# Optimization experiments

Measured on AMD Instinct MI355X. Metric: run time of the kernel, lower is better.

## Reference

```python
import jax, jax.numpy as jnp
import numpy as np

N_NODES = 100_000
N_EDGES = 1_600_000
F_IN = 128
HID = 64
C_OUT = 16


def setup_inputs() -> dict:
    key = jax.random.key(0)
    k1, k2, k3, k4, k5 = jax.random.split(key, 5)
    x = jax.random.normal(k1, (N_NODES, F_IN), dtype=jnp.float32)
    edge_index = jax.random.randint(k2, (2, N_EDGES), 0, N_NODES, dtype=jnp.int64)
    edge_weight = jax.random.uniform(k3, (N_EDGES,), dtype=jnp.float32)
    # Glorot-ish init for the two GCNConv linear layers; PyG inits bias to zero.
    W1 = jax.random.normal(k4, (F_IN, HID), dtype=jnp.float32) * (1.0 / np.sqrt(F_IN))
    b1 = jnp.zeros((HID,), dtype=jnp.float32)
    W2 = jax.random.normal(k5, (HID, C_OUT), dtype=jnp.float32) * (1.0 / np.sqrt(HID))
    b2 = jnp.zeros((C_OUT,), dtype=jnp.float32)
    return {"x": x, "edge_index": edge_index, "edge_weight": edge_weight,
            "W1": W1, "b1": b1, "W2": W2, "b2": b2}


def gcn_layer(x, row, col, ew, W, b, n):
    """PyG GCNConv: h = D^-1/2 (A + I) D^-1/2 (x W) + b, with edge weights.
    Self loops (weight 1) are handled analytically instead of appending edges."""
    h = x @ W  # [n, out]
    deg = jax.ops.segment_sum(ew, col, num_segments=n) + 1.0  # +1 for self loop
    dinv = jax.lax.rsqrt(deg)  # deg >= 1 always
    norm = dinv[row] * ew * dinv[col]  # [E]
    agg = jax.ops.segment_sum(norm[:, None] * h[row], col, num_segments=n)
    return agg + (dinv * dinv)[:, None] * h + b


def reference(x, edge_index, edge_weight, W1, b1, W2, b2):
    row, col = edge_index[0], edge_index[1]
    h = jax.nn.relu(gcn_layer(x, row, col, edge_weight, W1, b1, N_NODES))
    # delete_min_weighted_edges(node=0): remove the min-weight edge with source 0.
    # Zeroing its weight is mathematically identical to deleting it (it then
    # contributes 0 to both the degree and the aggregation).
    masked = jnp.where(row == 0, edge_weight, jnp.inf)
    idx = jnp.argmin(masked)
    ew2 = edge_weight.at[idx].set(0.0)
    return gcn_layer(h, row, col, ew2, W2, b2, N_NODES)
```

## Files before the change

### kernel.cpp

```cpp
#include <hip/hip_runtime.h>
#include <hip/hip_bf16.h>
#include <stdint.h>

#define NN 100000
#define NE 1600000
#define FIN 128
#define HID 64
#define COUT 16

#define BUKSH 8
#define NBUK ((NN + 255) >> BUKSH)
#define PART_NB 512
#define EPB (NE / PART_NB)
#define TSLCAP 5632

typedef unsigned long long u64;
typedef short bf16x8 __attribute__((ext_vector_type(8)));
typedef float f32x4 __attribute__((ext_vector_type(4)));

struct Flags { int f32; int i64; };

__device__ __forceinline__ float b2f(__hip_bfloat16 v) { return __bfloat162float(v); }

__device__ __forceinline__ float ldf(const void* p, size_t i, int f32) {
    return f32 ? ((const float*)p)[i]
               : __bfloat162float(((const __hip_bfloat16*)p)[i]);
}
__device__ __forceinline__ int lde(const void* p, size_t i, int i64) {
    return i64 ? (int)((const long long*)p)[i] : ((const int*)p)[i];
}
__device__ __forceinline__ void ld4bf(const __hip_bfloat16* p, float& x0, float& x1,
                                      float& x2, float& x3) {
    union { uint2 u; __hip_bfloat16 h[4]; } v;
    v.u = *(const uint2*)p;
    x0 = b2f(v.h[0]); x1 = b2f(v.h[1]); x2 = b2f(v.h[2]); x3 = b2f(v.h[3]);
}
__device__ __forceinline__ unsigned short f2bfu(float f) {
    union { __hip_bfloat16 b; unsigned short u; } c;
    c.b = __float2bfloat16(f);
    return c.u;
}
__device__ __forceinline__ float bfu2f(unsigned short u) {
    union { unsigned short h[2]; float f; } c;
    c.h[0] = 0; c.h[1] = u;
    return c.f;
}

__global__ __launch_bounds__(64) void k_init(const unsigned short* xs,
                                             const int* ei32, Flags* fl,
                                             u64* minkey, int* delpos,
                                             int* rowptrN) {
    int lane = threadIdx.x;
    int huge = 0;
    for (int i = lane * 2; i < 1024; i += 128) {
        int e = (xs[i] >> 7) & 0xFF;
        if (e >= 0xC0) huge = 1;
    }
    int odd_nonzero = 0;
    for (int i = 1 + lane * 2; i < 512; i += 128) {
        if (ei32[i] != 0) odd_nonzero = 1;
    }
    u64 h = __ballot(huge), o = __ballot(odd_nonzero);
    if (lane == 0) {
        fl->f32 = (h != 0); fl->i64 = (o == 0);
        *minkey = ~0ull;
        *delpos = 0x7fffffff;
        rowptrN[NN] = NE;
    }
}

__global__ __launch_bounds__(512) void k_hist(const void* __restrict__ ei,
                                              const void* __restrict__ ew,
                                              const Flags* __restrict__ fl,
                                              int* __restrict__ blockhist,
                                              u64* __restrict__ minkey) {
    __shared__ int cnt[NBUK];
    int b = blockIdx.x, t = threadIdx.x;
    int f32 = fl->f32, i64 = fl->i64;
    for (int i = t; i < NBUK; i += 512) cnt[i] = 0;
    __syncthreads();
    int e0 = b * EPB;
    for (int i = t; i < EPB; i += 512) {
        int e = e0 + i;
        int c = lde(ei, (size_t)NE + e, i64);
        atomicAdd(&cnt[c >> BUKSH], 1);
        int r = lde(ei, (size_t)e, i64);
        if (r == 0) {
            float w = ldf(ew, e, f32);
            u64 key = ((u64)__float_as_uint(w) << 32) | (unsigned)e;
            atomicMin(minkey, key);
        }
    }
    __syncthreads();
    for (int i = t; i < NBUK; i += 512)
        blockhist[(size_t)b * NBUK + i] = cnt[i];
}

__global__ __launch_bounds__(256) void k_scan1(const int* __restrict__ blockhist,
                                               int* __restrict__ buktotal) {
    __shared__ int sm[256];
    int i = blockIdx.x, t = threadIdx.x;
    int s = 0;
    for (int b = t; b < PART_NB; b += 256) s += blockhist[(size_t)b * NBUK + i];
    sm[t] = s;
    __syncthreads();
    for (int off = 128; off > 0; off >>= 1) {
        if (t < off) sm[t] += sm[t + off];
        __syncthreads();
    }
    if (t == 0) buktotal[i] = sm[0];
}

__global__ __launch_bounds__(512) void k_scan2(const int* __restrict__ blockhist,
                                               const int* __restrict__ buktotal,
                                               int* __restrict__ blockbase,
                                               int* __restrict__ bucketBaseArr) {
    __shared__ int pfx[512];
    __shared__ int bbs;
    int i = blockIdx.x, t = threadIdx.x;
    pfx[t] = (t < i && t < NBUK) ? buktotal[t] : 0;
    __syncthreads();
    for (int off = 256; off > 0; off >>= 1) {
        if (t < off) pfx[t] += pfx[t + off];
        __syncthreads();
    }
    if (t == 0) { bbs = pfx[0]; bucketBaseArr[i] = pfx[0]; }
    __syncthreads();
    int gbase = bbs;
    __syncthreads();
    int v = blockhist[(size_t)t * NBUK + i];
    pfx[t] = v;
    for (int off = 1; off < 512; off <<= 1) {
        __syncthreads();
        int add = (t >= off) ? pfx[t - off] : 0;
        __syncthreads();
        pfx[t] += add;
    }
    __syncthreads();
    blockbase[(size_t)t * NBUK + i] = gbase + pfx[t] - v;
}

__global__ __launch_bounds__(512) void k_scat(const void* __restrict__ ei,
                                              const void* __restrict__ ew,
                                              const Flags* __restrict__ fl,
                                              const int* __restrict__ blockbase,
                                              long long* __restrict__ tmp) {
    __shared__ int cnt[NBUK];
    int b = blockIdx.x, t = threadIdx.x;
    int f32 = fl->f32, i64 = fl->i64;
    for (int i = t; i < NBUK; i += 512) cnt[i] = 0;
    __syncthreads();
    int e0 = b * EPB;
    const int* bb = blockbase + (size_t)b * NBUK;
    for (int i = t; i < EPB; i += 512) {
        int e = e0 + i;
        int c = lde(ei, (size_t)NE + e, i64);
        int r = lde(ei, (size_t)e, i64);
        float w = ldf(ew, e, f32);
        int buk = c >> BUKSH;
        int local = atomicAdd(&cnt[buk], 1);
        int pos = bb[buk] + local;
        unsigned lo = (unsigned)r | (((unsigned)c & 255u) << 17);
        tmp[pos] = ((long long)__float_as_int(w) << 32) | lo;
    }
}

__global__ __launch_bounds__(512) void k_partB(const int* __restrict__ buktotal,
                                               const int* __restrict__ bucketBaseArr,
                                               const long long* __restrict__ tmp,
                                               int2* __restrict__ epack,
                                               int* __restrict__ rowptrN,
                                               const void* __restrict__ ei,
                                               const void* __restrict__ ew,
                                               const Flags* __restrict__ fl,
                                               const u64* __restrict__ minkey,
                                               float* __restrict__ dinv1,
                                               float* __restrict__ dinv2,
                                               int* __restrict__ delpos) {
    __shared__ long long tsl[TSLCAP];
    __shared__ int cnt[256];
    __shared__ int pfx[256];
    __shared__ u64 wsum[256];
    int b = blockIdx.x, t = threadIdx.x;
    int count = buktotal[b];
    int gbase = bucketBaseArr[b];
    const long long* ts = tmp + gbase;
    int stage = count < TSLCAP ? count : TSLCAP;
    for (int i = t; i < stage; i += 512) tsl[i] = ts[i];
    if (t < 256) { cnt[t] = 0; wsum[t] = 0; }
    __syncthreads();
    for (int i = t; i < count; i += 512) {
        long long pk = (i < TSLCAP) ? tsl[i] : ts[i];
        unsigned lo = (unsigned)pk;
        int nl = (int)((lo >> 17) & 255u);
        atomicAdd(&cnt[nl], 1);
        float w = __int_as_float((int)(pk >> 32));
        atomicAdd(&wsum[nl], (u64)((double)w * 4294967296.0));
    }
    __syncthreads();
    int v = 0;
    if (t < 256) { v = cnt[t]; pfx[t] = v; }
    for (int off = 1; off < 256; off <<= 1) {
        __syncthreads();
        int add = (t < 256 && t >= off) ? pfx[t - off] : 0;
        __syncthreads();
        if (t < 256) pfx[t] += add;
    }
    __syncthreads();
    u64 kk = *minkey;
    int eidx = (kk == ~0ull) ? 0 : (int)(kk & 0xffffffffu);
    int smin  = lde(ei, (size_t)eidx, fl->i64);
    int cmin  = lde(ei, (size_t)NE + eidx, fl->i64);
    int wminb = __float_as_int(ldf(ew, eidx, fl->f32));
    bool myb = (b == (cmin >> BUKSH));
    int clow = cmin & 255;
    if (t < 256) {
        int excl = pfx[t] - v;
        int node = (b << BUKSH) + t;
        if (node < NN) {
            rowptrN[node] = gbase + excl;
            float degv = (float)((double)wsum[t] * (1.0 / 4294967296.0));
            float d1 = degv + 1.0f;
            float d2 = d1 - ((node == cmin) ? __int_as_float(wminb) : 0.0f);
            dinv1[node] = rsqrtf(d1);
            dinv2[node] = rsqrtf(d2);
        }
        cnt[t] = gbase + excl;
    }
    __syncthreads();
    for (int i = t; i < count; i += 512) {
        long long pk = (i < TSLCAP) ? tsl[i] : ts[i];
        unsigned lo = (unsigned)pk;
        int nl = (int)((lo >> 17) & 255u);
        int pos = atomicAdd(&cnt[nl], 1);
        long long outpk = (pk & 0xFFFFFFFF00000000LL) | (lo & 0x1FFFFu);
        *(long long*)(epack + pos) = outpk;
        if (myb && nl == clow && (int)(lo & 0x1FFFFu) == smin
            && (int)(pk >> 32) == wminb)
            atomicMin(delpos, pos);
    }
}

__global__ __launch_bounds__(256, 3) void k_gemm1(const void* __restrict__ xv_,
                                                  const void* __restrict__ W1_,
                                                  const Flags* __restrict__ fl,
                                                  const float* __restrict__ dinv1,
                                                  __hip_bfloat16* __restrict__ h1) {
    __shared__ __align__(16) unsigned short Wbuf[16384];
    int t = threadIdx.x;
    int wave = t >> 6, lane = t & 63;
    int quad = lane >> 4, col = lane & 15;
    if (fl->f32) {
        const float* x  = (const float*)xv_;
        const float* W1 = (const float*)W1_;
        unsigned short* Whi = Wbuf;
        unsigned short* Wlo = Wbuf + 8192;
        for (int i = t; i < 8192; i += 256) {
            int k = i >> 6;
            int n = i & 63;
            int kc = k >> 5, kr = k & 31;
            int q = kr >> 3, j = kr & 7;
            int n0 = n >> 4, c2 = n & 15;
            float w = W1[i];
            unsigned short hi = f2bfu(w);
            unsigned short lo = f2bfu(w - bfu2f(hi));
            int idx = ((n0 << 4) + (kc << 2) + q) * 128 + c2 * 8 + j;
            Whi[idx] = hi;
            Wlo[idx] = lo;
        }
        __syncthreads();
        bf16x8 Bh[4][4];
#pragma unroll
        for (int n0 = 0; n0 < 4; ++n0)
#pragma unroll
            for (int kc = 0; kc < 4; ++kc)
                Bh[kc][n0] = *(const bf16x8*)&Whi[((n0 << 4) + (kc << 2) + quad) * 128 + col * 8];
        int tile0 = (blockIdx.x * 4 + wave) * 2;
#pragma unroll 1
        for (int i = 0; i < 2; ++i) {
            int node0 = (tile0 + i) * 16;
            if (node0 >= NN) return;
            const float* xp = x + (size_t)(node0 + col) * FIN + quad * 8;
            float4 xv[8];
#pragma unroll
            for (int kc = 0; kc < 4; ++kc) {
                xv[2 * kc]     = *(const float4*)(xp + kc * 32);
                xv[2 * kc + 1] = *(const float4*)(xp + kc * 32 + 4);
            }
            f32x4 a0 = {0.f, 0.f, 0.f, 0.f}, a1 = a0, a2 = a0, a3 = a0;
#pragma unroll
            for (int kc = 0; kc < 4; ++kc) {
                float fv[8];
                fv[0] = xv[2 * kc].x;     fv[1] = xv[2 * kc].y;
                fv[2] = xv[2 * kc].z;     fv[3] = xv[2 * kc].w;
                fv[4] = xv[2 * kc + 1].x; fv[5] = xv[2 * kc + 1].y;
                fv[6] = xv[2 * kc + 1].z; fv[7] = xv[2 * kc + 1].w;
                bf16x8 Ah, Al;
#pragma unroll
                for (int j = 0; j < 8; ++j) {
                    unsigned short hi = f2bfu(fv[j]);
                    Ah[j] = (short)hi;
                    Al[j] = (short)f2bfu(fv[j] - bfu2f(hi));
                }
                int lbase = ((kc << 2) + quad) * 128 + col * 8;
                bf16x8 Bl0 = *(const bf16x8*)&Wlo[lbase];
                bf16x8 Bl1 = *(const bf16x8*)&Wlo[(1 << 4) * 128 + lbase];
                bf16x8 Bl2 = *(const bf16x8*)&Wlo[(2 << 4) * 128 + lbase];
                bf16x8 Bl3 = *(const bf16x8*)&Wlo[(3 << 4) * 128 + lbase];
                a0 = __builtin_amdgcn_mfma_f32_16x16x32_bf16(Ah, Bh[kc][0], a0, 0, 0, 0);
                a0 = __builtin_amdgcn_mfma_f32_16x16x32_bf16(Al, Bh[kc][0], a0, 0, 0, 0);
                a0 = __builtin_amdgcn_mfma_f32_16x16x32_bf16(Ah, Bl0,      a0, 0, 0, 0);
                a1 = __builtin_amdgcn_mfma_f32_16x16x32_bf16(Ah, Bh[kc][1], a1, 0, 0, 0);
                a1 = __builtin_amdgcn_mfma_f32_16x16x32_bf16(Al, Bh[kc][1], a1, 0, 0, 0);
                a1 = __builtin_amdgcn_mfma_f32_16x16x32_bf16(Ah, Bl1,      a1, 0, 0, 0);
                a2 = __builtin_amdgcn_mfma_f32_16x16x32_bf16(Ah, Bh[kc][2], a2, 0, 0, 0);
                a2 = __builtin_amdgcn_mfma_f32_16x16x32_bf16(Al, Bh[kc][2], a2, 0, 0, 0);
                a2 = __builtin_amdgcn_mfma_f32_16x16x32_bf16(Ah, Bl2,      a2, 0, 0, 0);
                a3 = __builtin_amdgcn_mfma_f32_16x16x32_bf16(Ah, Bh[kc][3], a3, 0, 0, 0);
                a3 = __builtin_amdgcn_mfma_f32_16x16x32_bf16(Al, Bh[kc][3], a3, 0, 0, 0);
                a3 = __builtin_amdgcn_mfma_f32_16x16x32_bf16(Ah, Bl3,      a3, 0, 0, 0);
            }
            __hip_bfloat16* hp = h1 + (size_t)(node0 + quad * 4) * HID + col;
#pragma unroll
            for (int r = 0; r < 4; ++r) {
                float dsc = dinv1[node0 + quad * 4 + r];
                hp[(size_t)r * HID + 0]  = __float2bfloat16(a0[r] * dsc);
                hp[(size_t)r * HID + 16] = __float2bfloat16(a1[r] * dsc);
                hp[(size_t)r * HID + 32] = __float2bfloat16(a2[r] * dsc);
                hp[(size_t)r * HID + 48] = __float2bfloat16(a3[r] * dsc);
            }
        }
    } else {
        const __hip_bfloat16* x = (const __hip_bfloat16*)xv_;
        const unsigned short* W1 = (const unsigned short*)W1_;
        unsigned short* Wf = Wbuf;
        for (int i = t; i < 8192; i += 256) {
            int k = i >> 6;
            int n = i & 63;
            int kc = k >> 5, kr = k & 31;
            int q = kr >> 3, j = kr & 7;
            int n0 = n >> 4, c2 = n & 15;
            Wf[((((n0 << 2) | kc) << 2) | q) * 128 + c2 * 8 + j] = W1[i];
        }
        __syncthreads();
        bf16x8 B[4][4];
#pragma unroll
        for (int n0 = 0; n0 < 4; ++n0)
#pragma unroll
            for (int kc = 0; kc < 4; ++kc)
                B[kc][n0] = *(const bf16x8*)&Wf[((((n0 << 2) | kc) << 2) | quad) * 128 + col * 8];
        int tile0 = (blockIdx.x * 4 + wave) * 2;
#pragma unroll 1
        for (int i = 0; i < 2; ++i) {
            int node0 = (tile0 + i) * 16;
            if (node0 >= NN) return;
            const __hip_bfloat16* xp = x + (size_t)(node0 + col) * FIN + quad * 8;
            f32x4 a0 = {0.f, 0.f, 0.f, 0.f}, a1 = a0, a2 = a0, a3 = a0;
#pragma unroll
            for (int kc = 0; kc < 4; ++kc) {
                bf16x8 A = *(const bf16x8*)(xp + kc * 32);
                a0 = __builtin_amdgcn_mfma_f32_16x16x32_bf16(A, B[kc][0], a0, 0, 0, 0);
                a1 = __builtin_amdgcn_mfma_f32_16x16x32_bf16(A, B[kc][1], a1, 0, 0, 0);
                a2 = __builtin_amdgcn_mfma_f32_16x16x32_bf16(A, B[kc][2], a2, 0, 0, 0);
                a3 = __builtin_amdgcn_mfma_f32_16x16x32_bf16(A, B[kc][3], a3, 0, 0, 0);
            }
            __hip_bfloat16* hp = h1 + (size_t)(node0 + quad * 4) * HID + col;
#pragma unroll
            for (int r = 0; r < 4; ++r) {
                float dsc = dinv1[node0 + quad * 4 + r];
                hp[(size_t)r * HID + 0]  = __float2bfloat16(a0[r] * dsc);
                hp[(size_t)r * HID + 16] = __float2bfloat16(a1[r] * dsc);
                hp[(size_t)r * HID + 32] = __float2bfloat16(a2[r] * dsc);
                hp[(size_t)r * HID + 48] = __float2bfloat16(a3[r] * dsc);
            }
        }
    }
}

__global__ __launch_bounds__(256) void k_agg1(const int* __restrict__ rowptrN,
                                              const int2* __restrict__ epack,
                                              const float* __restrict__ dinv1,
                                              const __hip_bfloat16* __restrict__ h1,
                                              const void* __restrict__ b1,
                                              const void* __restrict__ W2,
                                              const Flags* __restrict__ fl,
                                              const float* __restrict__ dinv2,
                                              float* __restrict__ h2) {
    __shared__ float Ws[HID * COUT];
    __shared__ float obuf[16][68];
    int t = threadIdx.x;
    int f32 = fl->f32;
    for (int i = t; i < HID * COUT; i += 256) Ws[i] = ldf(W2, i, f32);
    int nn = t >> 4;
    int n = blockIdx.x * 16 + nn;
    int l = t & 15;
    int f = l * 4;
    int wbase = t & 48;
    float dn = dinv1[n];
    int p0 = rowptrN[n], p1 = rowptrN[n + 1];
    float a0 = 0.f, a1 = 0.f, a2 = 0.f, a3 = 0.f;
    for (int p = p0; p < p1; p += 16) {
        int idx = p + l;
        int2 ev = make_int2(0, 0);
        if (idx < p1) ev = epack[idx];
        float cw = __int_as_float(ev.y);
        int rj[16];
#pragma unroll
        for (int j = 0; j < 16; ++j)
            rj[j] = __shfl(ev.x, wbase + j);
        uint2 raw[16];
#pragma unroll
        for (int j = 0; j < 16; ++j)
            raw[j] = *(const uint2*)(h1 + (size_t)rj[j] * HID + f);
#pragma unroll
        for (int j = 0; j < 16; ++j) {
            float c = __shfl(cw, wbase + j);
            union { uint2 u; __hip_bfloat16 h[4]; } v; v.u = raw[j];
            a0 += c * b2f(v.h[0]);
            a1 += c * b2f(v.h[1]);
            a2 += c * b2f(v.h[2]);
            a3 += c * b2f(v.h[3]);
        }
    }
    float x0, x1, x2, x3;
    ld4bf(h1 + (size_t)n * HID + f, x0, x1, x2, x3);
    obuf[nn][f + 0] = fmaxf(dn * (a0 + x0) + ldf(b1, f + 0, f32), 0.f);
    obuf[nn][f + 1] = fmaxf(dn * (a1 + x1) + ldf(b1, f + 1, f32), 0.f);
    obuf[nn][f + 2] = fmaxf(dn * (a2 + x2) + ldf(b1, f + 2, f32), 0.f);
    obuf[nn][f + 3] = fmaxf(dn * (a3 + x3) + ldf(b1, f + 3, f32), 0.f);
    __syncthreads();
    int c = t & 15;
    const float* orow = obuf[nn];
    float acc = 0.f;
#pragma unroll 8
    for (int k = 0; k < HID; ++k)
        acc += orow[k] * Ws[k * COUT + c];
    h2[(size_t)n * COUT + c] = acc * dinv2[n];
}

__global__ __launch_bounds__(256) void k_agg2(const int* __restrict__ rowptrN,
                                              const int2* __restrict__ epack,
                                              const float* __restrict__ dinv2,
                                              const float* __restrict__ h2,
                                              const void* __restrict__ bias2,
                                              const Flags* __restrict__ fl,
                                              const int* __restrict__ delpos,
                                              void* __restrict__ out) {
    int t = threadIdx.x;
    int n = blockIdx.x * 64 + (t >> 2);
    if (n >= NN) return;
    int l = t & 3;
    int f = l * 4;
    int wbase = t & 60;
    int f32 = fl->f32;
    int dp = *delpos;
    float dn = dinv2[n];
    int p0 = rowptrN[n], p1 = rowptrN[n + 1];
    float a0 = 0.f, a1 = 0.f, a2 = 0.f, a3 = 0.f;
    for (int p = p0; p < p1; p += 8) {
        int iA = p + l, iB = p + 4 + l;
        int2 evA = make_int2(0, 0), evB = make_int2(0, 0);
        if (iA < p1) evA = epack[iA];
        if (iB < p1) evB = epack[iB];
        float cwA = (iA == dp) ? 0.f : __int_as_float(evA.y);
        float cwB = (iB == dp) ? 0.f : __int_as_float(evB.y);
        int rj[8];
#pragma unroll
        for (int j = 0; j < 4; ++j) {
            rj[j]     = __shfl(evA.x, wbase + j);
            rj[4 + j] = __shfl(evB.x, wbase + j);
        }
        float4 hv[8];
#pragma unroll
        for (int j = 0; j < 8; ++j)
            hv[j] = *(const float4*)(h2 + (size_t)rj[j] * COUT + f);
#pragma unroll
        for (int j = 0; j < 4; ++j) {
            float cA = __shfl(cwA, wbase + j);
            float cB = __shfl(cwB, wbase + j);
            a0 += cA * hv[j].x + cB * hv[4 + j].x;
            a1 += cA * hv[j].y + cB * hv[4 + j].y;
            a2 += cA * hv[j].z + cB * hv[4 + j].z;
            a3 += cA * hv[j].w + cB * hv[4 + j].w;
        }
    }
    const float4 hn = *(const float4*)(h2 + (size_t)n * COUT + f);
    float o0 = dn * (a0 + hn.x) + ldf(bias2, f + 0, f32);
    float o1 = dn * (a1 + hn.y) + ldf(bias2, f + 1, f32);
    float o2 = dn * (a2 + hn.z) + ldf(bias2, f + 2, f32);
    float o3 = dn * (a3 + hn.w) + ldf(bias2, f + 3, f32);
    size_t idx = (size_t)n * COUT + f;
    if (f32) {
        float* op = (float*)out + idx;
        op[0] = o0; op[1] = o1; op[2] = o2; op[3] = o3;
    } else {
        union { uint2 u; __hip_bfloat16 h[4]; } pk;
        pk.h[0] = __float2bfloat16(o0); pk.h[1] = __float2bfloat16(o1);
        pk.h[2] = __float2bfloat16(o2); pk.h[3] = __float2bfloat16(o3);
        *(uint2*)((__hip_bfloat16*)out + idx) = pk.u;
    }
}

extern "C" void kernel_launch(void* const* d_in, const int* in_sizes, int n_in,
                              void* d_out, int out_size, void* d_ws, size_t ws_size,
                              hipStream_t stream) {
    const void* x  = d_in[0];
    const void* ei = d_in[1];
    const void* ew = d_in[2];
    const void* W1 = d_in[3];
    const void* b1 = d_in[4];
    const void* W2 = d_in[5];
    const void* b2 = d_in[6];

    char* wsb = (char*)d_ws;
    int*   blockhist = (int*)wsb;                      wsb += (size_t)PART_NB * NBUK * 4;
    int*   blockbase = (int*)wsb;                      wsb += (size_t)PART_NB * NBUK * 4;
    int*   buktotal  = (int*)wsb;                      wsb += (size_t)NBUK * 4;
    int*   bucketBaseArr = (int*)wsb;                  wsb += (size_t)NBUK * 4;
    float* dinv1    = (float*)wsb;                     wsb += (size_t)NN * 4;
    float* dinv2    = (float*)wsb;                     wsb += (size_t)NN * 4;
    int*   rowptrN  = (int*)wsb;                       wsb += (size_t)(NN + 1) * 4;
    wsb = (char*)(((uintptr_t)wsb + 15) & ~(uintptr_t)15);
    int2*  epack    = (int2*)wsb;                      wsb += (size_t)NE * 8;
    __hip_bfloat16* h1 = (__hip_bfloat16*)wsb;         wsb += (size_t)NN * HID * 2;
    float* h2       = (float*)wsb;                     wsb += (size_t)NN * COUT * 4;
    long long* tmp  = (long long*)wsb;                 wsb += (size_t)NE * 8;
    u64*   minkey   = (u64*)wsb;                       wsb += 8;
    Flags* fl       = (Flags*)wsb;                     wsb += 8;
    int*   delpos   = (int*)wsb;                       wsb += 8;

    k_init<<<1, 64, 0, stream>>>((const unsigned short*)x, (const int*)ei, fl,
                                 minkey, delpos, rowptrN);
    k_hist<<<PART_NB, 512, 0, stream>>>(ei, ew, fl, blockhist, minkey);
    k_scan1<<<NBUK, 256, 0, stream>>>(blockhist, buktotal);
    k_scan2<<<NBUK, 512, 0, stream>>>(blockhist, buktotal, blockbase, bucketBaseArr);
    k_scat<<<PART_NB, 512, 0, stream>>>(ei, ew, fl, blockbase, tmp);
    k_partB<<<NBUK, 512, 0, stream>>>(buktotal, bucketBaseArr, tmp, epack, rowptrN,
                                      ei, ew, fl, minkey, dinv1, dinv2, delpos);
    k_gemm1<<<(NN / 16 + 7) / 8, 256, 0, stream>>>(x, W1, fl, dinv1, h1);
    k_agg1<<<NN / 16, 256, 0, stream>>>(rowptrN, epack, dinv1, h1, b1, W2, fl,
                                        dinv2, h2);
    k_agg2<<<(NN + 63) / 64, 256, 0, stream>>>(rowptrN, epack, dinv2, h2, b2, fl,
                                               delpos, d_out);
}
```

Before: 245.8 us.

## Fuse edge histogram with first-layer GEMM and move dinv scaling into aggregation

The first-layer GEMM no longer scales by dinv1 and is merged into the histogram kernel as extra blocks, so x@W1 runs concurrently with the edge-count pass instead of after the CSR build. The source-side dinv1 factor is now applied per edge in agg1 and the self-loop term gets dn twice. This removes one launch and overlaps compute-heavy GEMM with the memory-bound histogram. In exchange it adds a gather of dinv1 per edge in aggregation and raises the GEMM block size to 512 threads, which drops the previous launch bound of 3 blocks per unit.

```diff
diff --git a/kernel.cpp b/kernel.cpp
--- a/kernel.cpp
+++ b/kernel.cpp
@@ -12,6 +12,7 @@
 #define NBUK ((NN + 255) >> BUKSH)
 #define PART_NB 512
 #define EPB (NE / PART_NB)
+#define GEMM_NB ((NN / 16 + 15) / 16)
 #define TSLCAP 5632
 
 typedef unsigned long long u64;
@@ -69,185 +70,40 @@
     }
 }
 
-__global__ __launch_bounds__(512) void k_hist(const void* __restrict__ ei,
-                                              const void* __restrict__ ew,
-                                              const Flags* __restrict__ fl,
-                                              int* __restrict__ blockhist,
-                                              u64* __restrict__ minkey) {
+__global__ __launch_bounds__(512) void k_histgemm1(const void* __restrict__ ei,
+                                                   const void* __restrict__ ew,
+                                                   const Flags* __restrict__ fl,
+                                                   int* __restrict__ blockhist,
+                                                   u64* __restrict__ minkey,
+                                                   const void* __restrict__ xv_,
+                                                   const void* __restrict__ W1_,
+                                                   __hip_bfloat16* __restrict__ h1) {
     __shared__ int cnt[NBUK];
-    int b = blockIdx.x, t = threadIdx.x;
-    int f32 = fl->f32, i64 = fl->i64;
-    for (int i = t; i < NBUK; i += 512) cnt[i] = 0;
-    __syncthreads();
-    int e0 = b * EPB;
-    for (int i = t; i < EPB; i += 512) {
-        int e = e0 + i;
-        int c = lde(ei, (size_t)NE + e, i64);
-        atomicAdd(&cnt[c >> BUKSH], 1);
-        int r = lde(ei, (size_t)e, i64);
-        if (r == 0) {
-            float w = ldf(ew, e, f32);
-            u64 key = ((u64)__float_as_uint(w) << 32) | (unsigned)e;
-            atomicMin(minkey, key);
-        }
-    }
-    __syncthreads();
-    for (int i = t; i < NBUK; i += 512)
-        blockhist[(size_t)b * NBUK + i] = cnt[i];
-}
-
-__global__ __launch_bounds__(256) void k_scan1(const int* __restrict__ blockhist,
-                                               int* __restrict__ buktotal) {
-    __shared__ int sm[256];
-    int i = blockIdx.x, t = threadIdx.x;
-    int s = 0;
-    for (int b = t; b < PART_NB; b += 256) s += blockhist[(size_t)b * NBUK + i];
-    sm[t] = s;
-    __syncthreads();
-    for (int off = 128; off > 0; off >>= 1) {
-        if (t < off) sm[t] += sm[t + off];
-        __syncthreads();
-    }
-    if (t == 0) buktotal[i] = sm[0];
-}
-
-__global__ __launch_bounds__(512) void k_scan2(const int* __restrict__ blockhist,
-                                               const int* __restrict__ buktotal,
-                                               int* __restrict__ blockbase,
-                                               int* __restrict__ bucketBaseArr) {
-    __shared__ int pfx[512];
-    __shared__ int bbs;
-    int i = blockIdx.x, t = threadIdx.x;
-    pfx[t] = (t < i && t < NBUK) ? buktotal[t] : 0;
-    __syncthreads();
-    for (int off = 256; off > 0; off >>= 1) {
-        if (t < off) pfx[t] += pfx[t + off];
-        __syncthreads();
-    }
-    if (t == 0) { bbs = pfx[0]; bucketBaseArr[i] = pfx[0]; }
-    __syncthreads();
-    int gbase = bbs;
-    __syncthreads();
-    int v = blockhist[(size_t)t * NBUK + i];
-    pfx[t] = v;
-    for (int off = 1; off < 512; off <<= 1) {
-        __syncthreads();
-        int add = (t >= off) ? pfx[t - off] : 0;
-        __syncthreads();
-        pfx[t] += add;
-    }
-    __syncthreads();
-    blockbase[(size_t)t * NBUK + i] = gbase + pfx[t] - v;
-}
-
-__global__ __launch_bounds__(512) void k_scat(const void* __restrict__ ei,
-                                              const void* __restrict__ ew,
-                                              const Flags* __restrict__ fl,
-                                              const int* __restrict__ blockbase,
-                                              long long* __restrict__ tmp) {
-    __shared__ int cnt[NBUK];
-    int b = blockIdx.x, t = threadIdx.x;
-    int f32 = fl->f32, i64 = fl->i64;
-    for (int i = t; i < NBUK; i += 512) cnt[i] = 0;
-    __syncthreads();
-    int e0 = b * EPB;
-    const int* bb = blockbase + (size_t)b * NBUK;
-    for (int i = t; i < EPB; i += 512) {
-        int e = e0 + i;
-        int c = lde(ei, (size_t)NE + e, i64);
-        int r = lde(ei, (size_t)e, i64);
-        float w = ldf(ew, e, f32);
-        int buk = c >> BUKSH;
-        int local = atomicAdd(&cnt[buk], 1);
-        int pos = bb[buk] + local;
-        unsigned lo = (unsigned)r | (((unsigned)c & 255u) << 17);
-        tmp[pos] = ((long long)__float_as_int(w) << 32) | lo;
-    }
-}
-
-__global__ __launch_bounds__(512) void k_partB(const int* __restrict__ buktotal,
-                                               const int* __restrict__ bucketBaseArr,
-                                               const long long* __restrict__ tmp,
-                                               int2* __restrict__ epack,
-                                               int* __restrict__ rowptrN,
-                                               const void* __restrict__ ei,
-                                               const void* __restrict__ ew,
-                                               const Flags* __restrict__ fl,
-                                               const u64* __restrict__ minkey,
-                                               float* __restrict__ dinv1,
-                                               float* __restrict__ dinv2,
-                                               int* __restrict__ delpos) {
-    __shared__ long long tsl[TSLCAP];
-    __shared__ int cnt[256];
-    __shared__ int pfx[256];
-    __shared__ u64 wsum[256];
-    int b = blockIdx.x, t = threadIdx.x;
-    int count = buktotal[b];
-    int gbase = bucketBaseArr[b];
-    const long long* ts = tmp + gbase;
-    int stage = count < TSLCAP ? count : TSLCAP;
-    for (int i = t; i < stage; i += 512) tsl[i] = ts[i];
-    if (t < 256) { cnt[t] = 0; wsum[t] = 0; }
-    __syncthreads();
-    for (int i = t; i < count; i += 512) {
-        long long pk = (i < TSLCAP) ? tsl[i] : ts[i];
-        unsigned lo = (unsigned)pk;
-        int nl = (int)((lo >> 17) & 255u);
-        atomicAdd(&cnt[nl], 1);
-        float w = __int_as_float((int)(pk >> 32));
-        atomicAdd(&wsum[nl], (u64)((double)w * 4294967296.0));
-    }
-    __syncthreads();
-    int v = 0;
-    if (t < 256) { v = cnt[t]; pfx[t] = v; }
-    for (int off = 1; off < 256; off <<= 1) {
-        __syncthreads();
-        int add = (t < 256 && t >= off) ? pfx[t - off] : 0;
-        __syncthreads();
-        if (t < 256) pfx[t] += add;
-    }
-    __syncthreads();
-    u64 kk = *minkey;
-    int eidx = (kk == ~0ull) ? 0 : (int)(kk & 0xffffffffu);
-    int smin  = lde(ei, (size_t)eidx, fl->i64);
-    int cmin  = lde(ei, (size_t)NE + eidx, fl->i64);
-    int wminb = __float_as_int(ldf(ew, eidx, fl->f32));
-    bool myb = (b == (cmin >> BUKSH));
-    int clow = cmin & 255;
-    if (t < 256) {
-        int excl = pfx[t] - v;
-        int node = (b << BUKSH) + t;
-        if (node < NN) {
-            rowptrN[node] = gbase + excl;
-            float degv = (float)((double)wsum[t] * (1.0 / 4294967296.0));
-            float d1 = degv + 1.0f;
-            float d2 = d1 - ((node == cmin) ? __int_as_float(wminb) : 0.0f);
-            dinv1[node] = rsqrtf(d1);
-            dinv2[node] = rsqrtf(d2);
-        }
-        cnt[t] = gbase + excl;
-    }
-    __syncthreads();
-    for (int i = t; i < count; i += 512) {
-        long long pk = (i < TSLCAP) ? tsl[i] : ts[i];
-        unsigned lo = (unsigned)pk;
-        int nl = (int)((lo >> 17) & 255u);
-        int pos = atomicAdd(&cnt[nl], 1);
-        long long outpk = (pk & 0xFFFFFFFF00000000LL) | (lo & 0x1FFFFu);
-        *(long long*)(epack + pos) = outpk;
-        if (myb && nl == clow && (int)(lo & 0x1FFFFu) == smin
-            && (int)(pk >> 32) == wminb)
-            atomicMin(delpos, pos);
-    }
-}
-
-__global__ __launch_bounds__(256, 3) void k_gemm1(const void* __restrict__ xv_,
-                                                  const void* __restrict__ W1_,
-                                                  const Flags* __restrict__ fl,
-                                                  const float* __restrict__ dinv1,
-                                                  __hip_bfloat16* __restrict__ h1) {
     __shared__ __align__(16) unsigned short Wbuf[16384];
     int t = threadIdx.x;
+    if (blockIdx.x < PART_NB) {
+        int b = blockIdx.x;
+        int f32 = fl->f32, i64 = fl->i64;
+        for (int i = t; i < NBUK; i += 512) cnt[i] = 0;
+        __syncthreads();
+        int e0 = b * EPB;
+        for (int i = t; i < EPB; i += 512) {
+            int e = e0 + i;
+            int c = lde(ei, (size_t)NE + e, i64);
+            atomicAdd(&cnt[c >> BUKSH], 1);
+            int r = lde(ei, (size_t)e, i64);
+            if (r == 0) {
+                float w = ldf(ew, e, f32);
+                u64 key = ((u64)__float_as_uint(w) << 32) | (unsigned)e;
+                atomicMin(minkey, key);
+            }
+        }
+        __syncthreads();
+        for (int i = t; i < NBUK; i += 512)
+            blockhist[(size_t)b * NBUK + i] = cnt[i];
+        return;
+    }
+    int gb = blockIdx.x - PART_NB;
     int wave = t >> 6, lane = t & 63;
     int quad = lane >> 4, col = lane & 15;
     if (fl->f32) {
@@ -255,7 +111,7 @@
         const float* W1 = (const float*)W1_;
         unsigned short* Whi = Wbuf;
         unsigned short* Wlo = Wbuf + 8192;
-        for (int i = t; i < 8192; i += 256) {
+        for (int i = t; i < 8192; i += 512) {
             int k = i >> 6;
             int n = i & 63;
             int kc = k >> 5, kr = k & 31;
@@ -275,7 +131,7 @@
 #pragma unroll
             for (int kc = 0; kc < 4; ++kc)
                 Bh[kc][n0] = *(const bf16x8*)&Whi[((n0 << 4) + (kc << 2) + quad) * 128 + col * 8];
-        int tile0 = (blockIdx.x * 4 + wave) * 2;
+        int tile0 = (gb * 8 + wave) * 2;
 #pragma unroll 1
         for (int i = 0; i < 2; ++i) {
             int node0 = (tile0 + i) * 16;
@@ -323,18 +179,17 @@
             __hip_bfloat16* hp = h1 + (size_t)(node0 + quad * 4) * HID + col;
 #pragma unroll
             for (int r = 0; r < 4; ++r) {
-                float dsc = dinv1[node0 + quad * 4 + r];
-                hp[(size_t)r * HID + 0]  = __float2bfloat16(a0[r] * dsc);
-                hp[(size_t)r * HID + 16] = __float2bfloat16(a1[r] * dsc);
-                hp[(size_t)r * HID + 32] = __float2bfloat16(a2[r] * dsc);
-                hp[(size_t)r * HID + 48] = __float2bfloat16(a3[r] * dsc);
+                hp[(size_t)r * HID + 0]  = __float2bfloat16(a0[r]);
+                hp[(size_t)r * HID + 16] = __float2bfloat16(a1[r]);
+                hp[(size_t)r * HID + 32] = __float2bfloat16(a2[r]);
+                hp[(size_t)r * HID + 48] = __float2bfloat16(a3[r]);
             }
         }
     } else {
         const __hip_bfloat16* x = (const __hip_bfloat16*)xv_;
         const unsigned short* W1 = (const unsigned short*)W1_;
         unsigned short* Wf = Wbuf;
-        for (int i = t; i < 8192; i += 256) {
+        for (int i = t; i < 8192; i += 512) {
             int k = i >> 6;
             int n = i & 63;
             int kc = k >> 5, kr = k & 31;
@@ -349,7 +204,7 @@
 #pragma unroll
             for (int kc = 0; kc < 4; ++kc)
                 B[kc][n0] = *(const bf16x8*)&Wf[((((n0 << 2) | kc) << 2) | quad) * 128 + col * 8];
-        int tile0 = (blockIdx.x * 4 + wave) * 2;
+        int tile0 = (gb * 8 + wave) * 2;
 #pragma unroll 1
         for (int i = 0; i < 2; ++i) {
             int node0 = (tile0 + i) * 16;
@@ -367,13 +222,157 @@
             __hip_bfloat16* hp = h1 + (size_t)(node0 + quad * 4) * HID + col;
 #pragma unroll
             for (int r = 0; r < 4; ++r) {
-                float dsc = dinv1[node0 + quad * 4 + r];
-                hp[(size_t)r * HID + 0]  = __float2bfloat16(a0[r] * dsc);
-                hp[(size_t)r * HID + 16] = __float2bfloat16(a1[r] * dsc);
-                hp[(size_t)r * HID + 32] = __float2bfloat16(a2[r] * dsc);
-                hp[(size_t)r * HID + 48] = __float2bfloat16(a3[r] * dsc);
+                hp[(size_t)r * HID + 0]  = __float2bfloat16(a0[r]);
+                hp[(size_t)r * HID + 16] = __float2bfloat16(a1[r]);
+                hp[(size_t)r * HID + 32] = __float2bfloat16(a2[r]);
+                hp[(size_t)r * HID + 48] = __float2bfloat16(a3[r]);
             }
         }
+    }
+}
+
+__global__ __launch_bounds__(256) void k_scan1(const int* __restrict__ blockhist,
+                                               int* __restrict__ buktotal) {
+    __shared__ int sm[256];
+    int i = blockIdx.x, t = threadIdx.x;
+    int s = 0;
+    for (int b = t; b < PART_NB; b += 256) s += blockhist[(size_t)b * NBUK + i];
+    sm[t] = s;
+    __syncthreads();
+    for (int off = 128; off > 0; off >>= 1) {
+        if (t < off) sm[t] += sm[t + off];
+        __syncthreads();
+    }
+    if (t == 0) buktotal[i] = sm[0];
+}
+
+__global__ __launch_bounds__(512) void k_scan2(const int* __restrict__ blockhist,
+                                               const int* __restrict__ buktotal,
+                                               int* __restrict__ blockbase,
+                                               int* __restrict__ bucketBaseArr) {
+    __shared__ int pfx[512];
+    __shared__ int bbs;
+    int i = blockIdx.x, t = threadIdx.x;
+    pfx[t] = (t < i && t < NBUK) ? buktotal[t] : 0;
+    __syncthreads();
+    for (int off = 256; off > 0; off >>= 1) {
+        if (t < off) pfx[t] += pfx[t + off];
+        __syncthreads();
+    }
+    if (t == 0) { bbs = pfx[0]; bucketBaseArr[i] = pfx[0]; }
+    __syncthreads();
+    int gbase = bbs;
+    __syncthreads();
+    int v = blockhist[(size_t)t * NBUK + i];
+    pfx[t] = v;
+    for (int off = 1; off < 512; off <<= 1) {
+        __syncthreads();
+        int add = (t >= off) ? pfx[t - off] : 0;
+        __syncthreads();
+        pfx[t] += add;
+    }
+    __syncthreads();
+    blockbase[(size_t)t * NBUK + i] = gbase + pfx[t] - v;
+}
+
+__global__ __launch_bounds__(512) void k_scat(const void* __restrict__ ei,
+                                              const void* __restrict__ ew,
+                                              const Flags* __restrict__ fl,
+                                              const int* __restrict__ blockbase,
+                                              long long* __restrict__ tmp) {
+    __shared__ int cnt[NBUK];
+    int b = blockIdx.x, t = threadIdx.x;
+    int f32 = fl->f32, i64 = fl->i64;
+    for (int i = t; i < NBUK; i += 512) cnt[i] = 0;
+    __syncthreads();
+    int e0 = b * EPB;
+    const int* bb = blockbase + (size_t)b * NBUK;
+    for (int i = t; i < EPB; i += 512) {
+        int e = e0 + i;
+        int c = lde(ei, (size_t)NE + e, i64);
+        int r = lde(ei, (size_t)e, i64);
+        float w = ldf(ew, e, f32);
+        int buk = c >> BUKSH;
+        int local = atomicAdd(&cnt[buk], 1);
+        int pos = bb[buk] + local;
+        unsigned lo = (unsigned)r | (((unsigned)c & 255u) << 17);
+        tmp[pos] = ((long long)__float_as_int(w) << 32) | lo;
+    }
+}
+
+__global__ __launch_bounds__(512) void k_partB(const int* __restrict__ buktotal,
+                                               const int* __restrict__ bucketBaseArr,
+                                               const long long* __restrict__ tmp,
+                                               int2* __restrict__ epack,
+                                               int* __restrict__ rowptrN,
+                                               const void* __restrict__ ei,
+                                               const void* __restrict__ ew,
+                                               const Flags* __restrict__ fl,
+                                               const u64* __restrict__ minkey,
+                                               float* __restrict__ dinv1,
+                                               float* __restrict__ dinv2,
+                                               int* __restrict__ delpos) {
+    __shared__ long long tsl[TSLCAP];
+    __shared__ int cnt[256];
+    __shared__ int pfx[256];
+    __shared__ u64 wsum[256];
+    int b = blockIdx.x, t = threadIdx.x;
+    int count = buktotal[b];
+    int gbase = bucketBaseArr[b];
+    const long long* ts = tmp + gbase;
+    int stage = count < TSLCAP ? count : TSLCAP;
+    for (int i = t; i < stage; i += 512) tsl[i] = ts[i];
+    if (t < 256) { cnt[t] = 0; wsum[t] = 0; }
+    __syncthreads();
+    for (int i = t; i < count; i += 512) {
+        long long pk = (i < TSLCAP) ? tsl[i] : ts[i];
+        unsigned lo = (unsigned)pk;
+        int nl = (int)((lo >> 17) & 255u);
+        atomicAdd(&cnt[nl], 1);
+        float w = __int_as_float((int)(pk >> 32));
+        atomicAdd(&wsum[nl], (u64)((double)w * 4294967296.0));
+    }
+    __syncthreads();
+    int v = 0;
+    if (t < 256) { v = cnt[t]; pfx[t] = v; }
+    for (int off = 1; off < 256; off <<= 1) {
+        __syncthreads();
+        int add = (t < 256 && t >= off) ? pfx[t - off] : 0;
+        __syncthreads();
+        if (t < 256) pfx[t] += add;
+    }
+    __syncthreads();
+    u64 kk = *minkey;
+    int eidx = (kk == ~0ull) ? 0 : (int)(kk & 0xffffffffu);
+    int smin  = lde(ei, (size_t)eidx, fl->i64);
+    int cmin  = lde(ei, (size_t)NE + eidx, fl->i64);
+    int wminb = __float_as_int(ldf(ew, eidx, fl->f32));
+    bool myb = (b == (cmin >> BUKSH));
+    int clow = cmin & 255;
+    if (t < 256) {
+        int excl = pfx[t] - v;
+        int node = (b << BUKSH) + t;
+        if (node < NN) {
+            rowptrN[node] = gbase + excl;
+            float degv = (float)((double)wsum[t] * (1.0 / 4294967296.0));
+            float d1 = degv + 1.0f;
+            float d2 = d1 - ((node == cmin) ? __int_as_float(wminb) : 0.0f);
+            dinv1[node] = rsqrtf(d1);
+            dinv2[node] = rsqrtf(d2);
+        }
+        cnt[t] = gbase + excl;
+    }
+    __syncthreads();
+    for (int i = t; i < count; i += 512) {
+        long long pk = (i < TSLCAP) ? tsl[i] : ts[i];
+        unsigned lo = (unsigned)pk;
+        int nl = (int)((lo >> 17) & 255u);
+        int pos = atomicAdd(&cnt[nl], 1);
+        long long outpk = (pk & 0xFFFFFFFF00000000LL) | (lo & 0x1FFFFu);
+        *(long long*)(epack + pos) = outpk;
+        if (myb && nl == clow && (int)(lo & 0x1FFFFu) == smin
+            && (int)(pk >> 32) == wminb)
+            atomicMin(delpos, pos);
     }
 }
 
@@ -403,7 +402,7 @@
         int idx = p + l;
         int2 ev = make_int2(0, 0);
         if (idx < p1) ev = epack[idx];
-        float cw = __int_as_float(ev.y);
+        float cw = __int_as_float(ev.y) * dinv1[ev.x];
         int rj[16];
 #pragma unroll
         for (int j = 0; j < 16; ++j)
@@ -424,10 +423,10 @@
     }
     float x0, x1, x2, x3;
     ld4bf(h1 + (size_t)n * HID + f, x0, x1, x2, x3);
-    obuf[nn][f + 0] = fmaxf(dn * (a0 + x0) + ldf(b1, f + 0, f32), 0.f);
-    obuf[nn][f + 1] = fmaxf(dn * (a1 + x1) + ldf(b1, f + 1, f32), 0.f);
-    obuf[nn][f + 2] = fmaxf(dn * (a2 + x2) + ldf(b1, f + 2, f32), 0.f);
-    obuf[nn][f + 3] = fmaxf(dn * (a3 + x3) + ldf(b1, f + 3, f32), 0.f);
+    obuf[nn][f + 0] = fmaxf(dn * (a0 + dn * x0) + ldf(b1, f + 0, f32), 0.f);
+    obuf[nn][f + 1] = fmaxf(dn * (a1 + dn * x1) + ldf(b1, f + 1, f32), 0.f);
+    obuf[nn][f + 2] = fmaxf(dn * (a2 + dn * x2) + ldf(b1, f + 2, f32), 0.f);
+    obuf[nn][f + 3] = fmaxf(dn * (a3 + dn * x3) + ldf(b1, f + 3, f32), 0.f);
     __syncthreads();
     int c = t & 15;
     const float* orow = obuf[nn];
@@ -531,13 +530,13 @@
 
     k_init<<<1, 64, 0, stream>>>((const unsigned short*)x, (const int*)ei, fl,
                                  minkey, delpos, rowptrN);
-    k_hist<<<PART_NB, 512, 0, stream>>>(ei, ew, fl, blockhist, minkey);
+    k_histgemm1<<<PART_NB + GEMM_NB, 512, 0, stream>>>(ei, ew, fl, blockhist,
+                                                       minkey, x, W1, h1);
     k_scan1<<<NBUK, 256, 0, stream>>>(blockhist, buktotal);
     k_scan2<<<NBUK, 512, 0, stream>>>(blockhist, buktotal, blockbase, bucketBaseArr);
     k_scat<<<PART_NB, 512, 0, stream>>>(ei, ew, fl, blockbase, tmp);
     k_partB<<<NBUK, 512, 0, stream>>>(buktotal, bucketBaseArr, tmp, epack, rowptrN,
                                       ei, ew, fl, minkey, dinv1, dinv2, delpos);
-    k_gemm1<<<(NN / 16 + 7) / 8, 256, 0, stream>>>(x, W1, fl, dinv1, h1);
     k_agg1<<<NN / 16, 256, 0, stream>>>(rowptrN, epack, dinv1, h1, b1, W2, fl,
                                         dinv2, h2);
     k_agg2<<<(NN + 63) / 64, 256, 0, stream>>>(rowptrN, epack, dinv2, h2, b2, fl,
```

Measured after the change: 249.4 us. About the same (+1.4%).
